# Performance work log

Measured on AMD Instinct MI355X. Metric: run time of the kernel, lower is better.

The kernel has to match this reference:

```python
import jax, jax.numpy as jnp
import numpy as np
import math

N_NODES = 2000
LOOKBACK = 24
IN_DIM = 16
EMB_DIM = 64
BATCH = 32
LN_EPS = 1e-5


def _layernorm(v, g, b):
    mu = jnp.mean(v, axis=-1, keepdims=True)
    var = jnp.var(v, axis=-1, keepdims=True)
    return (v - mu) * jax.lax.rsqrt(var + LN_EPS) * g + b


def setup_inputs() -> dict:
    key = jax.random.key(0)
    ks = jax.random.split(key, 12)
    td = LOOKBACK * IN_DIM  # 384
    s_in = 1.0 / math.sqrt(td)
    s_d = 1.0 / math.sqrt(IN_DIM)
    return {
        "x": jax.random.normal(ks[0], (BATCH, N_NODES, LOOKBACK, IN_DIM), jnp.float32),
        "Wq": jax.random.normal(ks[1], (td, EMB_DIM), jnp.float32) * s_in,
        "bq": jax.random.normal(ks[2], (EMB_DIM,), jnp.float32) * 0.01,
        "Wk": jax.random.normal(ks[3], (td, EMB_DIM), jnp.float32) * s_in,
        "bk": jax.random.normal(ks[4], (EMB_DIM,), jnp.float32) * 0.01,
        "g0": jnp.ones((EMB_DIM,), jnp.float32),
        "beta0": jnp.zeros((EMB_DIM,), jnp.float32),
        "g1": jnp.ones((EMB_DIM,), jnp.float32),
        "beta1": jnp.zeros((EMB_DIM,), jnp.float32),
        "normal": jax.random.normal(ks[5], (N_NODES, LOOKBACK, IN_DIM), jnp.float32),
        "Win": jax.random.normal(ks[6], (IN_DIM, IN_DIM), jnp.float32) * s_d,
    }


def reference(x, Wq, bq, Wk, bk, g0, beta0, g1, beta1, normal, Win):
    b, n, t, d = x.shape
    xf = x.reshape(b, n, t * d)
    # per-sample q/k linear + layernorm (batched over b)
    q1 = _layernorm(xf @ Wq + bq, g0, beta0)  # (b, n, e)
    k1 = _layernorm(xf @ Wk + bk, g1, beta1)  # (b, n, e)
    # node-mixing attention: softmax(q k^T / sqrt(num_nodes)) @ normal
    scores = jnp.einsum('bne,bme->bnm', q1, k1) / math.sqrt(n)
    A = jax.nn.softmax(scores, axis=-1)  # (b, n, n)
    data = jnp.einsum('bnm,mf->bnf', A, normal.reshape(n, t * d)).reshape(b, n, t, d)
    # RPPsAtt attention weights over time (general attention, output_len = 1)
    query = x[:, :, -1, :] @ Win  # (b, n, d)
    att = jnp.einsum('bnd,bntd->bnt', query, data)  # scores vs context
    weight = jax.nn.softmax(att, axis=-1)  # (b, n, t)
    # res = stack(weights).permute(0,1,3,2) -> (b, n, t, 1), broadcast-add
    return data + weight[..., None]
```

## Files before the change

### kernel.cpp

```cpp
#include <hip/hip_runtime.h>
#include <math.h>

#define B_   32
#define NN   2000
#define NP   2048
#define TT   24
#define TD   384
#define EE   64
#define SCALE 0.022360679774997896f

typedef __bf16 bf16;
typedef __bf16 bf16x8 __attribute__((ext_vector_type(8)));
typedef float  f32x4  __attribute__((ext_vector_type(4)));

typedef __attribute__((address_space(3))) unsigned int       lds_u32;
typedef const __attribute__((address_space(1))) unsigned int g_u32;

__device__ __forceinline__ void dma16(const void* g, void* l) {
    __builtin_amdgcn_global_load_lds((g_u32*)g, (lds_u32*)l, 16, 0, 0);
}

__device__ __forceinline__ bool input_is_bf16(const void* g0) {
    return *reinterpret_cast<const unsigned short*>(g0) == 0x3F80;
}

__device__ __forceinline__ float safexp(float v) {
    return __expf(fminf(fmaxf(v, -30.f), 30.f));
}

__device__ __forceinline__ bf16x8 ld_frag(const bf16* p) {
    return *reinterpret_cast<const bf16x8*>(p);
}

__device__ __forceinline__ bf16x8 cvt8_f32(const float* p) {
    f32x4 a = *reinterpret_cast<const f32x4*>(p);
    f32x4 b = *reinterpret_cast<const f32x4*>(p + 4);
    bf16x8 r;
    r[0]=(bf16)a[0]; r[1]=(bf16)a[1]; r[2]=(bf16)a[2]; r[3]=(bf16)a[3];
    r[4]=(bf16)b[0]; r[5]=(bf16)b[1]; r[6]=(bf16)b[2]; r[7]=(bf16)b[3];
    return r;
}

__global__ void pack_w_k(const void* Wqv, const void* Wkv, bf16* __restrict__ Wp,
                         const void* gflag) {
    bool bf = input_is_bf16(gflag);
    int o = blockIdx.x * 256 + threadIdx.x;
    if (o >= 12*8*64*8) return;
    int j  = o & 7;
    int l  = (o >> 3) & 63;
    int nt = (o >> 9) & 7;
    int ks = o >> 12;
    int k   = ks*32 + ((l >> 4) * 8) + j;
    int col = nt*16 + (l & 15);
    float v;
    if (bf) v = (col < 64) ? (float)((const bf16*)Wqv)[k*64 + col]
                           : (float)((const bf16*)Wkv)[k*64 + col - 64];
    else    v = (col < 64) ? ((const float*)Wqv)[k*64 + col]
                           : ((const float*)Wkv)[k*64 + col - 64];
    Wp[o] = (bf16)v;
}

__global__ void pack_v_k(const void* normalv, bf16* __restrict__ Vp, const void* gflag) {
    bool bf = input_is_bf16(gflag);
    int o = blockIdx.x * 256 + threadIdx.x;
    if (o >= 64*24*512) return;
    int j  = o & 7;
    int l  = (o >> 3) & 63;
    int nt = (o >> 9) % 24;
    int kb = o / (24*512);
    int key = kb*32 + ((l >> 4) * 8) + j;
    int col = nt*16 + (l & 15);
    float v = 0.f;
    if (key < NN)
        v = bf ? (float)((const bf16*)normalv)[key*TD + col]
               : ((const float*)normalv)[key*TD + col];
    Vp[o] = (bf16)v;
}

__global__ void calc_query_k(const void* xv, const void* Winv, float* __restrict__ Qry,
                             const void* gflag) {
    bool bf = input_is_bf16(gflag);
    int o = blockIdx.x * 256 + threadIdx.x;
    if (o >= B_*NP*16) return;
    int d2 = o & 15;
    int n  = (o >> 4) & (NP - 1);
    int b  = o >> 15;
    float acc = 0.f;
    if (n < NN) {
        size_t xoff = ((size_t)(b*NN + n))*TD + (TT-1)*16;
        if (bf) {
            const bf16* xr = (const bf16*)xv + xoff;
            const bf16* Wn = (const bf16*)Winv;
            #pragma unroll
            for (int d = 0; d < 16; ++d) acc += (float)xr[d] * (float)Wn[d*16 + d2];
        } else {
            const float* xr = (const float*)xv + xoff;
            const float* Wn = (const float*)Winv;
            #pragma unroll
            for (int d = 0; d < 16; ++d) acc += xr[d] * Wn[d*16 + d2];
        }
    }
    Qry[o] = acc;
}

__global__ __launch_bounds__(256) void proj_ln_k(
        const void* xv, const bf16* __restrict__ Wp,
        const void* bqv, const void* bkv,
        const void* g0v, const void* be0v,
        const void* g1v, const void* be1v,
        bf16* __restrict__ Qb, bf16* __restrict__ Kp) {
    __shared__ __align__(16) bf16 Wbuf[2][4096];
    bool bf = input_is_bf16(g0v);
    int mb = blockIdx.x, b = blockIdx.y;
    int w    = threadIdx.x >> 6;
    int lane = threadIdx.x & 63;
    int quad = lane >> 4, lq = lane & 15;

    int rowA = mb*64 + w*16 + lq;
    int xrow = rowA < NN ? rowA : NN - 1;

    bf16x8 afr[12];
    if (bf) {
        const bf16* xp = (const bf16*)xv + ((size_t)(b*NN + xrow))*TD + quad*8;
        #pragma unroll
        for (int ks = 0; ks < 12; ++ks) afr[ks] = ld_frag(xp + ks*32);
    } else {
        const float* xp = (const float*)xv + ((size_t)(b*NN + xrow))*TD + quad*8;
        #pragma unroll
        for (int ks = 0; ks < 12; ++ks) afr[ks] = cvt8_f32(xp + ks*32);
    }

    auto stage = [&](int ks, int bufi) {
        const char* g = (const char*)Wp + (size_t)ks*8192;
        for (int c = w; c < 8; c += 4)
            dma16(g + c*1024 + (size_t)lane*16, &Wbuf[bufi][c*512]);
    };
    stage(0, 0);

    f32x4 acc[8];
    #pragma unroll
    for (int nt = 0; nt < 8; ++nt) acc[nt] = (f32x4){0.f, 0.f, 0.f, 0.f};
    __syncthreads();

    for (int ks = 0; ks < 12; ++ks) {
        int cur = ks & 1;
        if (ks + 1 < 12) stage(ks + 1, cur ^ 1);
        const bf16* wb = Wbuf[cur];
        #pragma unroll
        for (int nt = 0; nt < 8; ++nt) {
            bf16x8 bfr = ld_frag(wb + nt*512 + lane*8);
            acc[nt] = __builtin_amdgcn_mfma_f32_16x16x32_bf16(afr[ks], bfr, acc[nt], 0, 0, 0);
        }
        __syncthreads();
    }

    #pragma unroll
    for (int nt = 0; nt < 8; ++nt) {
        int c = nt*16 + lq;
        float bias;
        if (bf) bias = (c < 64) ? (float)((const bf16*)bqv)[c] : (float)((const bf16*)bkv)[c-64];
        else    bias = (c < 64) ? ((const float*)bqv)[c] : ((const float*)bkv)[c-64];
        #pragma unroll
        for (int r = 0; r < 4; ++r) acc[nt][r] += bias;
    }
    float outn[8][4];
    #pragma unroll
    for (int g = 0; g < 2; ++g) {
        float s[4], sq[4];
        #pragma unroll
        for (int r = 0; r < 4; ++r) {
            float p = 0.f, p2 = 0.f;
            #pragma unroll
            for (int nt = 0; nt < 4; ++nt) {
                float v = acc[g*4 + nt][r];
                p += v; p2 += v*v;
            }
            s[r] = p; sq[r] = p2;
        }
        #pragma unroll
        for (int m = 1; m < 16; m <<= 1) {
            #pragma unroll
            for (int r = 0; r < 4; ++r) {
                s[r]  += __shfl_xor(s[r],  m, 16);
                sq[r] += __shfl_xor(sq[r], m, 16);
            }
        }
        #pragma unroll
        for (int r = 0; r < 4; ++r) {
            float mean = s[r] * (1.f/64.f);
            float var  = fmaxf(sq[r] * (1.f/64.f) - mean*mean, 0.f);
            float rs   = rsqrtf(var + 1e-5f);
            #pragma unroll
            for (int nt = 0; nt < 4; ++nt) {
                int c = nt*16 + lq;
                float gv, bv;
                if (g == 0) { gv = bf ? (float)((const bf16*)g0v)[c] : ((const float*)g0v)[c];
                              bv = bf ? (float)((const bf16*)be0v)[c] : ((const float*)be0v)[c]; }
                else        { gv = bf ? (float)((const bf16*)g1v)[c] : ((const float*)g1v)[c];
                              bv = bf ? (float)((const bf16*)be1v)[c] : ((const float*)be1v)[c]; }
                outn[g*4 + nt][r] = (acc[g*4 + nt][r] - mean) * rs * gv + bv;
            }
        }
    }
    int rowq = mb*64 + w*16 + quad*4;
    #pragma unroll
    for (int r = 0; r < 4; ++r) {
        int row = rowq + r;
        bool real = row < NN;
        size_t qbase = ((size_t)(b*NP + row))*EE;
        int kb2  = row >> 5;
        int half = (row >> 4) & 1;
        int lqk  = row & 15;
        #pragma unroll
        for (int nt = 0; nt < 4; ++nt) {
            Qb[qbase + nt*16 + lq] = (bf16)(real ? outn[nt][r] : 0.f);
            int col   = nt*16 + lq;
            int f     = half*2 + (col >> 5);
            int quadk = (col >> 3) & 3;
            size_t idx = (((size_t)(b*64 + kb2)*4 + f)*64 + quadk*16 + lqk)*8 + (col & 7);
            Kp[idx] = (bf16)(real ? outn[4 + nt][r] : 0.f);
        }
    }
}

__global__ __launch_bounds__(512, 4) void attn_k(
        const bf16* __restrict__ Qb, const bf16* __restrict__ Kp,
        const bf16* __restrict__ Vp, const float* __restrict__ Qry,
        void* outv, const void* gflag) {
    __shared__ __align__(16) char SM[61440];
    bf16*  Kb    = (bf16*)(SM);
    bf16*  Vb    = (bf16*)(SM + 8192);
    bf16*  Pl    = (bf16*)(SM + 57344);
    bf16*  scr   = (bf16*)(SM);
    float* eBuf  = (float*)(SM + 52224);
    float* denP  = (float*)(SM + 58880);
    float* dnInv = (float*)(SM + 59392);

    bool bf = input_is_bf16(gflag);
    int mb = blockIdx.x, b = blockIdx.y;
    int w    = threadIdx.x >> 6;
    int lane = threadIdx.x & 63;
    int quad = lane >> 4, lq = lane & 15;
    int rowbase = mb*64;
    int rt = w >> 1;
    int h  = w & 1;

    const bf16* qp = Qb + ((size_t)(b*NP + rowbase + rt*16 + lq))*EE + quad*8;
    bf16x8 aq0 = ld_frag(qp);
    bf16x8 aq1 = ld_frag(qp + 32);

    f32x4 acc[4][3];
    #pragma unroll
    for (int i = 0; i < 4; ++i)
        #pragma unroll
        for (int ct = 0; ct < 3; ++ct) acc[i][ct] = (f32x4){0.f, 0.f, 0.f, 0.f};
    float den[4] = {0.f, 0.f, 0.f, 0.f};

    const bf16* kg = Kp + (size_t)(b*64)*2048;
    auto stage = [&](int kb, int bufi) {
        const char* kgb = (const char*)(kg + (size_t)kb*2048);
        const char* vgb = (const char*)(Vp + (size_t)kb*12288);
        for (int c = w; c < 28; c += 8) {
            if (c < 4) dma16(kgb + c*1024 + (size_t)lane*16, Kb + bufi*2048 + c*512);
            else       dma16(vgb + (size_t)(c-4)*1024 + (size_t)lane*16,
                             Vb + bufi*12288 + (c-4)*512);
        }
    };
    stage(0, 0);
    __syncthreads();

    for (int kb = 0; kb < 63; ++kb) {
        int cur = kb & 1;
        if (kb + 1 < 63) stage(kb + 1, cur ^ 1);

        const bf16* kc = Kb + cur*2048 + h*1024;
        bf16x8 bk0 = ld_frag(kc + lane*8);
        bf16x8 bk1 = ld_frag(kc + 512 + lane*8);
        f32x4 s = (f32x4){0.f,0.f,0.f,0.f};
        s = __builtin_amdgcn_mfma_f32_16x16x32_bf16(aq0, bk0, s, 0, 0, 0);
        s = __builtin_amdgcn_mfma_f32_16x16x32_bf16(aq1, bk1, s, 0, 0, 0);

        int kok = (kb*32 + h*16 + lq) < NN;
        bf16* pw = Pl + rt*512;
        int pb = (h*2 + (lq >> 3))*128 + quad*32 + (lq & 7);
        #pragma unroll
        for (int r = 0; r < 4; ++r) {
            float e = safexp(s[r] * SCALE);
            den[r] += kok ? e : 0.f;
            pw[pb + r*8] = (bf16)e;
        }

        const bf16* vc = Vb + cur*12288 + (w*3)*512;
        bf16x8 bv0 = ld_frag(vc + lane*8);
        bf16x8 bv1 = ld_frag(vc +  512 + lane*8);
        bf16x8 bv2 = ld_frag(vc + 1024 + lane*8);

        asm volatile("s_waitcnt lgkmcnt(0)" ::: "memory");
        __builtin_amdgcn_s_barrier();
        asm volatile("" ::: "memory");
        __builtin_amdgcn_sched_barrier(0);

        #pragma unroll
        for (int rt2 = 0; rt2 < 4; ++rt2) {
            bf16x8 ap = ld_frag(Pl + rt2*512 + lane*8);
            acc[rt2][0] = __builtin_amdgcn_mfma_f32_16x16x32_bf16(ap, bv0, acc[rt2][0], 0, 0, 0);
            acc[rt2][1] = __builtin_amdgcn_mfma_f32_16x16x32_bf16(ap, bv1, acc[rt2][1], 0, 0, 0);
            acc[rt2][2] = __builtin_amdgcn_mfma_f32_16x16x32_bf16(ap, bv2, acc[rt2][2], 0, 0, 0);
        }
        __syncthreads();
    }

    #pragma unroll
    for (int r = 0; r < 4; ++r) {
        float s = den[r];
        s += __shfl_xor(s, 1, 16); s += __shfl_xor(s, 2, 16);
        s += __shfl_xor(s, 4, 16); s += __shfl_xor(s, 8, 16);
        den[r] = s;
    }
    if (lq == 0) {
        #pragma unroll
        for (int r = 0; r < 4; ++r) denP[h*64 + rt*16 + quad*4 + r] = den[r];
    }
    __syncthreads();

    const float* qryb = Qry + ((size_t)(b*NP + rowbase))*16 + lq;
    #pragma unroll
    for (int rt2 = 0; rt2 < 4; ++rt2) {
        float inv[4], qd[4];
        #pragma unroll
        for (int r = 0; r < 4; ++r) {
            int row = rt2*16 + quad*4 + r;
            inv[r] = 1.f / fmaxf(denP[row] + denP[64 + row], 1e-30f);
            qd[r]  = qryb[(size_t)row*16];
        }
        #pragma unroll
        for (int ct = 0; ct < 3; ++ct) {
            #pragma unroll
            for (int r = 0; r < 4; ++r) {
                float v = acc[rt2][ct][r] * inv[r];
                acc[rt2][ct][r] = v;
                float a = v * qd[r];
                a += __shfl_xor(a, 1, 16); a += __shfl_xor(a, 2, 16);
                a += __shfl_xor(a, 4, 16); a += __shfl_xor(a, 8, 16);
                float e = safexp(a);
                if (lq == 0) eBuf[(rt2*16 + quad*4 + r)*26 + (w*3 + ct)] = e;
            }
        }
    }
    __syncthreads();

    if (lane < 8) {
        int row = w*8 + lane;
        float s = 0.f;
        #pragma unroll
        for (int t = 0; t < 24; ++t) s += eBuf[row*26 + t];
        dnInv[row] = 1.f / fmaxf(s, 1e-30f);
    }
    __syncthreads();

    if (bf) {
        #pragma unroll
        for (int rt2 = 0; rt2 < 4; ++rt2) {
            #pragma unroll
            for (int ct = 0; ct < 3; ++ct) {
                int t = w*3 + ct;
                #pragma unroll
                for (int r = 0; r < 4; ++r) {
                    int row = rt2*16 + quad*4 + r;
                    float wv = eBuf[row*26 + t] * dnInv[row];
                    scr[(size_t)row*408 + t*16 + lq] = (bf16)(acc[rt2][ct][r] + wv);
                }
            }
        }
        __syncthreads();
        bf16* og = (bf16*)outv + ((size_t)b*NN + rowbase)*TD;
        #pragma unroll
        for (int i = 0; i < 8; ++i) {
            int lrow = w*8 + i;
            int grow = rowbase + lrow;
            if (grow < NN && lane < 48)
                *reinterpret_cast<bf16x8*>(og + (size_t)lrow*TD + lane*8) =
                    *reinterpret_cast<const bf16x8*>(scr + (size_t)lrow*408 + lane*8);
        }
    } else {
        #pragma unroll
        for (int rt2 = 0; rt2 < 4; ++rt2) {
            #pragma unroll
            for (int ct = 0; ct < 3; ++ct) {
                int t = w*3 + ct;
                #pragma unroll
                for (int r = 0; r < 4; ++r) {
                    int row  = rt2*16 + quad*4 + r;
                    int grow = rowbase + row;
                    if (grow < NN) {
                        float wv = eBuf[row*26 + t] * dnInv[row];
                        ((float*)outv)[((size_t)(b*NN + grow))*TD + t*16 + lq] =
                            acc[rt2][ct][r] + wv;
                    }
                }
            }
        }
    }
}

extern "C" void kernel_launch(void* const* d_in, const int* in_sizes, int n_in,
                              void* d_out, int out_size, void* d_ws, size_t ws_size,
                              hipStream_t stream) {
    const void* x      = d_in[0];
    const void* Wq     = d_in[1];
    const void* bq     = d_in[2];
    const void* Wk     = d_in[3];
    const void* bk     = d_in[4];
    const void* g0     = d_in[5];
    const void* be0    = d_in[6];
    const void* g1     = d_in[7];
    const void* be1    = d_in[8];
    const void* normal = d_in[9];
    const void* Win    = d_in[10];

    char* ws = (char*)d_ws;
    bf16*  Qb  = (bf16*)(ws);
    bf16*  Kp  = (bf16*)(ws + 8388608);
    bf16*  Vp  = (bf16*)(ws + 16777216);
    bf16*  Wp  = (bf16*)(ws + 16777216 + 1638400);
    float* Qry = (float*)(ws + 16777216 + 1638400 + 98304);

    pack_w_k<<<dim3(192), dim3(256), 0, stream>>>(Wq, Wk, Wp, g0);
    pack_v_k<<<dim3(3072), dim3(256), 0, stream>>>(normal, Vp, g0);
    calc_query_k<<<dim3(4096), dim3(256), 0, stream>>>(x, Win, Qry, g0);
    proj_ln_k<<<dim3(32, 32), dim3(256), 0, stream>>>(x, Wp, bq, bk, g0, be0, g1, be1, Qb, Kp);
    attn_k<<<dim3(32, 32), dim3(512), 0, stream>>>(Qb, Kp, Vp, Qry, d_out, g0);
}
```

Measured before the change: 387.1 us.

## Software-pipeline attention loop so P·V overlaps next QK and halves barriers

Restructures the attention main loop into a prologue/steady-state/epilogue pipeline. The QK scores and exp for block kb are computed while the P·V MFMAs consume the previous block's probabilities from a double-buffered P tile, removing the mid-iteration barrier so each iteration has one sync. DMA staging is made branch-free with precomputed per-wave offsets and advancing pointers. The key-validity mask is specialised into the last iteration only. Shared memory grows to 64KB, and the new buffer offsets (the second P buffer sits near denP/dnInv) need to stay non-overlapping, which could hurt occupancy or correctness.

After: 379.4 us. 2.0% less time.

```diff
diff --git a/kernel.cpp b/kernel.cpp
--- a/kernel.cpp
+++ b/kernel.cpp
@@ -227,14 +227,13 @@
         const bf16* __restrict__ Qb, const bf16* __restrict__ Kp,
         const bf16* __restrict__ Vp, const float* __restrict__ Qry,
         void* outv, const void* gflag) {
-    __shared__ __align__(16) char SM[61440];
-    bf16*  Kb    = (bf16*)(SM);
-    bf16*  Vb    = (bf16*)(SM + 8192);
-    bf16*  Pl    = (bf16*)(SM + 57344);
-    bf16*  scr   = (bf16*)(SM);
-    float* eBuf  = (float*)(SM + 52224);
-    float* denP  = (float*)(SM + 58880);
-    float* dnInv = (float*)(SM + 59392);
+    __shared__ __align__(16) char SM[65536];
+    char* SMb = SM;
+    bf16*  PlB   = (bf16*)(SMb + 57344);
+    bf16*  scr   = (bf16*)(SMb);
+    float* eBuf  = (float*)(SMb + 52224);
+    float* denP  = (float*)(SMb + 58880);
+    float* dnInv = (float*)(SMb + 59392);
 
     bool bf = input_is_bf16(gflag);
     int mb = blockIdx.x, b = blockIdx.y;
@@ -256,59 +255,104 @@
         for (int ct = 0; ct < 3; ++ct) acc[i][ct] = (f32x4){0.f, 0.f, 0.f, 0.f};
     float den[4] = {0.f, 0.f, 0.f, 0.f};
 
-    const bf16* kg = Kp + (size_t)(b*64)*2048;
-    auto stage = [&](int kb, int bufi) {
-        const char* kgb = (const char*)(kg + (size_t)kb*2048);
-        const char* vgb = (const char*)(Vp + (size_t)kb*12288);
-        for (int c = w; c < 28; c += 8) {
-            if (c < 4) dma16(kgb + c*1024 + (size_t)lane*16, Kb + bufi*2048 + c*512);
-            else       dma16(vgb + (size_t)(c-4)*1024 + (size_t)lane*16,
-                             Vb + bufi*12288 + (c-4)*512);
-        }
+    const char* kSrc = (const char*)(Kp + (size_t)(b*64)*2048);
+    const char* vSrc = (const char*)Vp;
+    const int kOff  = w*1024 + lane*16;
+    const int jA = (w < 4) ? w + 4  : w - 4;
+    const int jB = (w < 4) ? w + 12 : w + 4;
+    const int jC = (w < 4) ? w + 20 : w + 12;
+    const int vOffA = jA*1024 + lane*16;
+    const int vOffB = jB*1024 + lane*16;
+    const int vOffC = jC*1024 + lane*16;
+
+    auto stage = [&](int bufi) {
+        char* kd = SMb + bufi*4096;
+        char* vd = SMb + 8192 + bufi*24576;
+        if (w < 4) dma16(kSrc + kOff, kd + w*1024);
+        dma16(vSrc + vOffA, vd + jA*1024);
+        dma16(vSrc + vOffB, vd + jB*1024);
+        dma16(vSrc + vOffC, vd + jC*1024);
+        kSrc += 4096; vSrc += 24576;
     };
-    stage(0, 0);
-    __syncthreads();
-
-    for (int kb = 0; kb < 63; ++kb) {
-        int cur = kb & 1;
-        if (kb + 1 < 63) stage(kb + 1, cur ^ 1);
-
-        const bf16* kc = Kb + cur*2048 + h*1024;
+
+    const int pb = (h*2 + (lq >> 3))*128 + quad*32 + (lq & 7);
+    auto do_qk = [&](int cur) -> f32x4 {
+        const bf16* kc = (const bf16*)(SMb + cur*4096) + h*1024;
         bf16x8 bk0 = ld_frag(kc + lane*8);
         bf16x8 bk1 = ld_frag(kc + 512 + lane*8);
         f32x4 s = (f32x4){0.f,0.f,0.f,0.f};
         s = __builtin_amdgcn_mfma_f32_16x16x32_bf16(aq0, bk0, s, 0, 0, 0);
         s = __builtin_amdgcn_mfma_f32_16x16x32_bf16(aq1, bk1, s, 0, 0, 0);
-
-        int kok = (kb*32 + h*16 + lq) < NN;
-        bf16* pw = Pl + rt*512;
-        int pb = (h*2 + (lq >> 3))*128 + quad*32 + (lq & 7);
-        #pragma unroll
-        for (int r = 0; r < 4; ++r) {
-            float e = safexp(s[r] * SCALE);
-            den[r] += kok ? e : 0.f;
-            pw[pb + r*8] = (bf16)e;
-        }
-
-        const bf16* vc = Vb + cur*12288 + (w*3)*512;
-        bf16x8 bv0 = ld_frag(vc + lane*8);
-        bf16x8 bv1 = ld_frag(vc +  512 + lane*8);
-        bf16x8 bv2 = ld_frag(vc + 1024 + lane*8);
-
-        asm volatile("s_waitcnt lgkmcnt(0)" ::: "memory");
-        __builtin_amdgcn_s_barrier();
-        asm volatile("" ::: "memory");
-        __builtin_amdgcn_sched_barrier(0);
-
+        return s;
+    };
+
+    bf16x8 bv0, bv1, bv2;
+    auto load_bv = [&](int cur) {
+        const bf16* vc = (const bf16*)(SMb + 8192 + cur*24576) + w*3*512;
+        bv0 = ld_frag(vc + lane*8);
+        bv1 = ld_frag(vc +  512 + lane*8);
+        bv2 = ld_frag(vc + 1024 + lane*8);
+    };
+    auto do_pv = [&](int pbuf) {
+        const bf16* pl = PlB + pbuf*2048;
         #pragma unroll
         for (int rt2 = 0; rt2 < 4; ++rt2) {
-            bf16x8 ap = ld_frag(Pl + rt2*512 + lane*8);
+            bf16x8 ap = ld_frag(pl + rt2*512 + lane*8);
             acc[rt2][0] = __builtin_amdgcn_mfma_f32_16x16x32_bf16(ap, bv0, acc[rt2][0], 0, 0, 0);
             acc[rt2][1] = __builtin_amdgcn_mfma_f32_16x16x32_bf16(ap, bv1, acc[rt2][1], 0, 0, 0);
             acc[rt2][2] = __builtin_amdgcn_mfma_f32_16x16x32_bf16(ap, bv2, acc[rt2][2], 0, 0, 0);
         }
+    };
+
+    stage(0);
+    __syncthreads();
+
+    {
+        f32x4 s = do_qk(0);
+        bf16* pw = PlB + rt*512;
+        #pragma unroll
+        for (int r = 0; r < 4; ++r) {
+            float e = safexp(s[r] * SCALE);
+            den[r] += e;
+            pw[pb + r*8] = (bf16)e;
+        }
+        stage(1);
+        load_bv(0);
         __syncthreads();
     }
+
+    for (int kb = 1; kb < 62; ++kb) {
+        int cur = kb & 1;
+        stage(cur ^ 1);
+        f32x4 s = do_qk(cur);
+        bf16* pw = PlB + cur*2048 + rt*512;
+        #pragma unroll
+        for (int r = 0; r < 4; ++r) {
+            float e = safexp(s[r] * SCALE);
+            den[r] += e;
+            pw[pb + r*8] = (bf16)e;
+        }
+        do_pv(cur ^ 1);
+        load_bv(cur);
+        __syncthreads();
+    }
+
+    {
+        f32x4 s = do_qk(0);
+        bf16* pw = PlB + rt*512;
+        #pragma unroll
+        for (int r = 0; r < 4; ++r) {
+            float e = safexp(s[r] * SCALE);
+            if (h == 0) den[r] += e;
+            pw[pb + r*8] = (bf16)e;
+        }
+        do_pv(1);
+        load_bv(0);
+        __syncthreads();
+    }
+
+    do_pv(0);
+    __syncthreads();
 
     #pragma unroll
     for (int r = 0; r < 4; ++r) {
```

## Load K/V fragments directly to registers and shrink LDS footprint

Applied to the files above, without the earlier changes.

Removes the LDS staging of K and V tiles via global_load_lds. Each wave now loads its K/V fragments straight from global memory into registers, software-pipelined two blocks ahead, with the P tile double-buffered in LDS so only one barrier per step remains. The bf16 output staging is split into two halves to cut shared memory from 60KB to about 41KB, which can raise occupancy. The cost is that each wave issues its own global loads, so data shared across waves is no longer loaded once, and register pressure goes up. Padding masking now relies on the final block's h==1 half being entirely pad rows.

Result: faster. 352.2 us (-9.0%).

```diff
diff --git a/kernel.cpp b/kernel.cpp
--- a/kernel.cpp
+++ b/kernel.cpp
@@ -227,14 +227,12 @@
         const bf16* __restrict__ Qb, const bf16* __restrict__ Kp,
         const bf16* __restrict__ Vp, const float* __restrict__ Qry,
         void* outv, const void* gflag) {
-    __shared__ __align__(16) char SM[61440];
-    bf16*  Kb    = (bf16*)(SM);
-    bf16*  Vb    = (bf16*)(SM + 8192);
-    bf16*  Pl    = (bf16*)(SM + 57344);
-    bf16*  scr   = (bf16*)(SM);
-    float* eBuf  = (float*)(SM + 52224);
-    float* denP  = (float*)(SM + 58880);
-    float* dnInv = (float*)(SM + 59392);
+    __shared__ __align__(16) char SM[41728];
+    bf16*  PlB   = (bf16*)(SM);
+    bf16*  scr   = (bf16*)(SM + 8192);
+    float* eBuf  = (float*)(SM + 34304);
+    float* denP  = (float*)(SM + 40960);
+    float* dnInv = (float*)(SM + 41472);
 
     bool bf = input_is_bf16(gflag);
     int mb = blockIdx.x, b = blockIdx.y;
@@ -256,59 +254,77 @@
         for (int ct = 0; ct < 3; ++ct) acc[i][ct] = (f32x4){0.f, 0.f, 0.f, 0.f};
     float den[4] = {0.f, 0.f, 0.f, 0.f};
 
-    const bf16* kg = Kp + (size_t)(b*64)*2048;
-    auto stage = [&](int kb, int bufi) {
-        const char* kgb = (const char*)(kg + (size_t)kb*2048);
-        const char* vgb = (const char*)(Vp + (size_t)kb*12288);
-        for (int c = w; c < 28; c += 8) {
-            if (c < 4) dma16(kgb + c*1024 + (size_t)lane*16, Kb + bufi*2048 + c*512);
-            else       dma16(vgb + (size_t)(c-4)*1024 + (size_t)lane*16,
-                             Vb + bufi*12288 + (c-4)*512);
-        }
+    const bf16* kg = Kp + (size_t)(b*64)*2048 + h*1024 + lane*8;
+    const bf16* vg = Vp + (size_t)(w*3)*512 + lane*8;
+
+    const int pb = (h*2 + (lq >> 3))*128 + quad*32 + (lq & 7);
+
+    auto barrier_p = [&]() {
+        asm volatile("s_waitcnt lgkmcnt(0)" ::: "memory");
+        __builtin_amdgcn_s_barrier();
+        __builtin_amdgcn_sched_barrier(0);
     };
-    stage(0, 0);
-    __syncthreads();
-
-    for (int kb = 0; kb < 63; ++kb) {
-        int cur = kb & 1;
-        if (kb + 1 < 63) stage(kb + 1, cur ^ 1);
-
-        const bf16* kc = Kb + cur*2048 + h*1024;
-        bf16x8 bk0 = ld_frag(kc + lane*8);
-        bf16x8 bk1 = ld_frag(kc + 512 + lane*8);
+    auto qk = [&](bf16x8 k0, bf16x8 k1) -> f32x4 {
         f32x4 s = (f32x4){0.f,0.f,0.f,0.f};
-        s = __builtin_amdgcn_mfma_f32_16x16x32_bf16(aq0, bk0, s, 0, 0, 0);
-        s = __builtin_amdgcn_mfma_f32_16x16x32_bf16(aq1, bk1, s, 0, 0, 0);
-
-        int kok = (kb*32 + h*16 + lq) < NN;
-        bf16* pw = Pl + rt*512;
-        int pb = (h*2 + (lq >> 3))*128 + quad*32 + (lq & 7);
+        s = __builtin_amdgcn_mfma_f32_16x16x32_bf16(aq0, k0, s, 0, 0, 0);
+        s = __builtin_amdgcn_mfma_f32_16x16x32_bf16(aq1, k1, s, 0, 0, 0);
+        return s;
+    };
+    auto emit_p = [&](f32x4 s, int buf, bool maskpad) {
+        bf16* pw = PlB + buf*2048 + rt*512;
         #pragma unroll
         for (int r = 0; r < 4; ++r) {
             float e = safexp(s[r] * SCALE);
-            den[r] += kok ? e : 0.f;
+            if (!maskpad || h == 0) den[r] += e;
             pw[pb + r*8] = (bf16)e;
         }
-
-        const bf16* vc = Vb + cur*12288 + (w*3)*512;
-        bf16x8 bv0 = ld_frag(vc + lane*8);
-        bf16x8 bv1 = ld_frag(vc +  512 + lane*8);
-        bf16x8 bv2 = ld_frag(vc + 1024 + lane*8);
-
-        asm volatile("s_waitcnt lgkmcnt(0)" ::: "memory");
-        __builtin_amdgcn_s_barrier();
-        asm volatile("" ::: "memory");
-        __builtin_amdgcn_sched_barrier(0);
-
+    };
+    auto pv = [&](int buf, bf16x8 v0, bf16x8 v1, bf16x8 v2) {
+        const bf16* pl = PlB + buf*2048;
         #pragma unroll
         for (int rt2 = 0; rt2 < 4; ++rt2) {
-            bf16x8 ap = ld_frag(Pl + rt2*512 + lane*8);
-            acc[rt2][0] = __builtin_amdgcn_mfma_f32_16x16x32_bf16(ap, bv0, acc[rt2][0], 0, 0, 0);
-            acc[rt2][1] = __builtin_amdgcn_mfma_f32_16x16x32_bf16(ap, bv1, acc[rt2][1], 0, 0, 0);
-            acc[rt2][2] = __builtin_amdgcn_mfma_f32_16x16x32_bf16(ap, bv2, acc[rt2][2], 0, 0, 0);
-        }
-        __syncthreads();
-    }
+            bf16x8 ap = ld_frag(pl + rt2*512 + lane*8);
+            acc[rt2][0] = __builtin_amdgcn_mfma_f32_16x16x32_bf16(ap, v0, acc[rt2][0], 0, 0, 0);
+            acc[rt2][1] = __builtin_amdgcn_mfma_f32_16x16x32_bf16(ap, v1, acc[rt2][1], 0, 0, 0);
+            acc[rt2][2] = __builtin_amdgcn_mfma_f32_16x16x32_bf16(ap, v2, acc[rt2][2], 0, 0, 0);
+        }
+    };
+
+    bf16x8 kA0 = ld_frag(kg), kA1 = ld_frag(kg + 512); kg += 2048;
+    bf16x8 kB0 = ld_frag(kg), kB1 = ld_frag(kg + 512); kg += 2048;
+    bf16x8 vB0 = ld_frag(vg), vB1 = ld_frag(vg + 512), vB2 = ld_frag(vg + 1024);
+    vg += 12288;
+    emit_p(qk(kA0, kA1), 0, false);
+    barrier_p();
+
+    for (int it = 0; it < 30; ++it) {
+        kA0 = ld_frag(kg); kA1 = ld_frag(kg + 512); kg += 2048;
+        bf16x8 vA0 = ld_frag(vg), vA1 = ld_frag(vg + 512), vA2 = ld_frag(vg + 1024);
+        vg += 12288;
+        pv(0, vB0, vB1, vB2);
+        emit_p(qk(kB0, kB1), 1, false);
+        barrier_p();
+        kB0 = ld_frag(kg); kB1 = ld_frag(kg + 512); kg += 2048;
+        vB0 = ld_frag(vg); vB1 = ld_frag(vg + 512); vB2 = ld_frag(vg + 1024);
+        vg += 12288;
+        pv(1, vA0, vA1, vA2);
+        emit_p(qk(kA0, kA1), 0, false);
+        barrier_p();
+    }
+
+    {
+        kA0 = ld_frag(kg); kA1 = ld_frag(kg + 512);
+        bf16x8 vA0 = ld_frag(vg), vA1 = ld_frag(vg + 512), vA2 = ld_frag(vg + 1024);
+        vg += 12288;
+        pv(0, vB0, vB1, vB2);
+        emit_p(qk(kB0, kB1), 1, false);
+        barrier_p();
+        vB0 = ld_frag(vg); vB1 = ld_frag(vg + 512); vB2 = ld_frag(vg + 1024);
+        pv(1, vA0, vA1, vA2);
+        emit_p(qk(kA0, kA1), 0, true);
+        barrier_p();
+    }
+    pv(0, vB0, vB1, vB2);
 
     #pragma unroll
     for (int r = 0; r < 4; ++r) {
@@ -360,27 +376,33 @@
 
     if (bf) {
         #pragma unroll
-        for (int rt2 = 0; rt2 < 4; ++rt2) {
-            #pragma unroll
-            for (int ct = 0; ct < 3; ++ct) {
-                int t = w*3 + ct;
+        for (int half = 0; half < 2; ++half) {
+            #pragma unroll
+            for (int rti = 0; rti < 2; ++rti) {
+                int rt2 = half*2 + rti;
                 #pragma unroll
-                for (int r = 0; r < 4; ++r) {
-                    int row = rt2*16 + quad*4 + r;
-                    float wv = eBuf[row*26 + t] * dnInv[row];
-                    scr[(size_t)row*408 + t*16 + lq] = (bf16)(acc[rt2][ct][r] + wv);
+                for (int ct = 0; ct < 3; ++ct) {
+                    int t = w*3 + ct;
+                    #pragma unroll
+                    for (int r = 0; r < 4; ++r) {
+                        int row = rt2*16 + quad*4 + r;
+                        float wv = eBuf[row*26 + t] * dnInv[row];
+                        scr[(size_t)(row - half*32)*408 + t*16 + lq] =
+                            (bf16)(acc[rt2][ct][r] + wv);
+                    }
                 }
             }
-        }
-        __syncthreads();
-        bf16* og = (bf16*)outv + ((size_t)b*NN + rowbase)*TD;
-        #pragma unroll
-        for (int i = 0; i < 8; ++i) {
-            int lrow = w*8 + i;
-            int grow = rowbase + lrow;
-            if (grow < NN && lane < 48)
-                *reinterpret_cast<bf16x8*>(og + (size_t)lrow*TD + lane*8) =
-                    *reinterpret_cast<const bf16x8*>(scr + (size_t)lrow*408 + lane*8);
+            __syncthreads();
+            bf16* og = (bf16*)outv + ((size_t)b*NN + rowbase + half*32)*TD;
+            #pragma unroll
+            for (int i = 0; i < 4; ++i) {
+                int lrow = w*4 + i;
+                int grow = rowbase + half*32 + lrow;
+                if (grow < NN && lane < 48)
+                    *reinterpret_cast<bf16x8*>(og + (size_t)lrow*TD + lane*8) =
+                        *reinterpret_cast<const bf16x8*>(scr + (size_t)lrow*408 + lane*8);
+            }
+            __syncthreads();
         }
     } else {
         #pragma unroll
```
